# Kernel tuning notes

Measured on AMD Instinct MI355X. Metric: run time of the kernel, lower is better.

Reference implementation:

```python
import jax, jax.numpy as jnp
import numpy as np

TOKENS = 8192
HIDDEN = 6144
NUM_EXPERTS = 768  # n_routed_experts (512) + zero_expert_num (256)
TOP_K = 12
ROUTED_SCALING_FACTOR = 2.5


def setup_inputs() -> dict:
    key = jax.random.key(0)
    k1, k2, k3 = jax.random.split(key, 3)
    hidden_states = jax.random.normal(k1, (TOKENS, HIDDEN), dtype=jnp.float32)
    classifier_weight = jax.random.normal(k2, (NUM_EXPERTS, HIDDEN), dtype=jnp.float32) * (1.0 / np.sqrt(HIDDEN))
    e_score_correction_bias = jax.random.normal(k3, (NUM_EXPERTS,), dtype=jnp.float32) * 0.1
    return {
        "hidden_states": hidden_states,
        "classifier_weight": classifier_weight,
        "e_score_correction_bias": e_score_correction_bias,
    }


def reference(hidden_states, classifier_weight, e_score_correction_bias):
    # [T, H] -> router logits [T, E] in fp32 (source casts to float32)
    x = hidden_states.reshape(-1, HIDDEN).astype(jnp.float32)
    router_logits = jnp.einsum('th,eh->te', x, classifier_weight)

    # npu_moe_gating_top_k(renorm=0, norm_type=0): softmax scores,
    # bias-corrected selection, gather un-biased scores, scale.
    scores = jax.nn.softmax(router_logits, axis=-1)                # [T, E]
    scores_for_choice = scores + e_score_correction_bias[None, :]  # [T, E]
    _, topk_indices = jax.lax.top_k(scores_for_choice, TOP_K)       # [T, K]
    topk_weights = jnp.take_along_axis(scores, topk_indices, axis=-1)
    topk_weights = topk_weights * ROUTED_SCALING_FACTOR

    return topk_indices.astype(jnp.int32), topk_weights
```

## Files before the change

### kernel.cpp

```cpp
#include <hip/hip_runtime.h>

#define TOKENS  8192
#define HIDDEN  6144
#define EXPERTS 768
#define TOPK    12
#define RSF     2.5f
#define ROWH    (HIDDEN * 2)

typedef float    f4 __attribute__((ext_vector_type(4)));
typedef _Float16 h8 __attribute__((ext_vector_type(8)));
typedef _Float16 h2 __attribute__((ext_vector_type(2)));
typedef __fp16   g2 __attribute__((ext_vector_type(2)));

#define BM 128
#define BN 96
#define BK 32
#define NKT (HIDDEN / BK)
#define BUFH 14336
#define LOH  7168
#define LO_SCALE 4096.0f
#define LO_INV   2.44140625e-4f

static __device__ inline h2 pk(float a, float b) {
    g2 r = __builtin_amdgcn_cvt_pkrtz(a, b);
    return __builtin_bit_cast(h2, r);
}

static __device__ inline void cvt8(const f4 a, const f4 b, h8& hi, h8& lo) {
    h2 ha = pk(a.x, a.y), hb = pk(a.z, a.w), hc = pk(b.x, b.y), hd = pk(b.z, b.w);
    h2 la = pk((a.x - (float)ha[0]) * LO_SCALE, (a.y - (float)ha[1]) * LO_SCALE);
    h2 lb = pk((a.z - (float)hb[0]) * LO_SCALE, (a.w - (float)hb[1]) * LO_SCALE);
    h2 lc = pk((b.x - (float)hc[0]) * LO_SCALE, (b.y - (float)hc[1]) * LO_SCALE);
    h2 ld = pk((b.z - (float)hd[0]) * LO_SCALE, (b.w - (float)hd[1]) * LO_SCALE);
    hi[0]=ha[0]; hi[1]=ha[1]; hi[2]=hb[0]; hi[3]=hb[1];
    hi[4]=hc[0]; hi[5]=hc[1]; hi[6]=hd[0]; hi[7]=hd[1];
    lo[0]=la[0]; lo[1]=la[1]; lo[2]=lb[0]; lo[3]=lb[1];
    lo[4]=lc[0]; lo[5]=lc[1]; lo[6]=ld[0]; lo[7]=ld[1];
}

__global__ __launch_bounds__(256)
void split_convert(float* __restrict__ X, float* __restrict__ W) {
    const size_t GX = (size_t)TOKENS * HIDDEN / 8;
    const size_t GW = (size_t)EXPERTS * HIDDEN / 8;
    size_t gid = (size_t)blockIdx.x * 256 + threadIdx.x;
    if (gid >= GX + GW) return;
    float* base; size_t loc;
    if (gid < GX) { base = X; loc = gid; } else { base = W; loc = gid - GX; }
    const f4* p = (const f4*)(base + loc * 8);
    f4 a = p[0], b = p[1];
    h8 hi, lo;
    cvt8(a, b, hi, lo);
    h8* o = (h8*)(base + loc * 8);
    o[0] = hi; o[1] = lo;
}

typedef __attribute__((address_space(1))) const void av1;
typedef __attribute__((address_space(3))) void av3;
static __device__ inline void stage16(const void* g, void* l) {
    __builtin_amdgcn_global_load_lds((av1*)g, (av3*)l, 16, 0, 0);
}

__global__ __launch_bounds__(256, 2)
void router_gemm(const _Float16* __restrict__ Xs, const _Float16* __restrict__ Ws,
                 float* __restrict__ L) {
    __shared__ _Float16 sm[2 * BUFH];

    const int t    = threadIdx.x;
    const int bm   = blockIdx.y * BM;
    const int bn   = blockIdx.x * BN;
    const int lane = t & 63;
    const int w    = t >> 6;
    const int lr   = lane & 15;
    const int lq   = lane >> 4;

    const _Float16* ps[7];
    uint32_t        ldso[7];
#pragma unroll
    for (int q = 0; q < 7; ++q) {
        const int j    = w * 7 + q;
        const int isLo = (j >= 14);
        const int jj   = isLo ? j - 14 : j;
        const int r    = jj * 16 + (lane >> 2);
        const int p    = lane & 3;
        const int g    = p ^ (r & 3);
        const _Float16* row = (r < BM) ? (Xs + (size_t)(bm + r) * ROWH)
                                       : (Ws + (size_t)(bn + r - BM) * ROWH);
        ps[q]   = row + g * 16 + isLo * 8;
        ldso[q] = (uint32_t)(isLo * LOH + jj * 512);
    }

    uint32_t aoff[4], boff[3];
#pragma unroll
    for (int mi = 0; mi < 4; ++mi) {
        const int r = (w & 1) * 64 + mi * 16 + lr;
        aoff[mi] = r * 32 + ((lq ^ (r & 3)) * 8);
    }
#pragma unroll
    for (int ni = 0; ni < 3; ++ni) {
        const int r = 128 + (w >> 1) * 48 + ni * 16 + lr;
        boff[ni] = r * 32 + ((lq ^ (r & 3)) * 8);
    }

    f4 acc_h[4][3], acc_c[4][3];
#pragma unroll
    for (int i = 0; i < 4; ++i)
#pragma unroll
        for (int j = 0; j < 3; ++j) { acc_h[i][j] = f4{0,0,0,0}; acc_c[i][j] = f4{0,0,0,0}; }

#pragma unroll
    for (int q = 0; q < 7; ++q) {
        stage16((const void*)ps[q], (void*)(sm + ldso[q]));
        ps[q] += 64;
    }

    auto do_tile = [&](const uint32_t boR, const uint32_t boW, const bool doStage) {
        if (doStage) {
#pragma unroll
            for (int q = 0; q < 7; ++q) {
                stage16((const void*)ps[q], (void*)(sm + boW + ldso[q]));
                ps[q] += 64;
            }
        }
        h8 ah[4], al[4], bh[3], bl[3];
#pragma unroll
        for (int mi = 0; mi < 4; ++mi) {
            ah[mi] = *(const h8*)(sm + boR + aoff[mi]);
            al[mi] = *(const h8*)(sm + boR + aoff[mi] + LOH);
        }
#pragma unroll
        for (int ni = 0; ni < 3; ++ni) {
            bh[ni] = *(const h8*)(sm + boR + boff[ni]);
            bl[ni] = *(const h8*)(sm + boR + boff[ni] + LOH);
        }
#pragma unroll
        for (int mi = 0; mi < 4; ++mi)
#pragma unroll
            for (int ni = 0; ni < 3; ++ni) {
                acc_h[mi][ni] = __builtin_amdgcn_mfma_f32_16x16x32_f16(ah[mi], bh[ni], acc_h[mi][ni], 0, 0, 0);
                acc_c[mi][ni] = __builtin_amdgcn_mfma_f32_16x16x32_f16(ah[mi], bl[ni], acc_c[mi][ni], 0, 0, 0);
                acc_c[mi][ni] = __builtin_amdgcn_mfma_f32_16x16x32_f16(al[mi], bh[ni], acc_c[mi][ni], 0, 0, 0);
            }
    };

    for (int T2 = 0; T2 < NKT / 2; ++T2) {
        __syncthreads();
        do_tile(0u, (uint32_t)BUFH, true);
        __syncthreads();
        do_tile((uint32_t)BUFH, 0u, T2 != NKT / 2 - 1);
    }

#pragma unroll
    for (int mi = 0; mi < 4; ++mi)
#pragma unroll
        for (int ni = 0; ni < 3; ++ni)
#pragma unroll
            for (int r = 0; r < 4; ++r) {
                const int gm = bm + (w & 1) * 64 + mi * 16 + lq * 4 + r;
                const int gn = bn + (w >> 1) * 48 + ni * 16 + lr;
                L[(size_t)gm * EXPERTS + gn] = acc_h[mi][ni][r] + acc_c[mi][ni][r] * LO_INV;
            }
}

__global__ __launch_bounds__(256)
void router_topk(const float* __restrict__ L, const float* __restrict__ bias,
                 float* __restrict__ outIdx, float* __restrict__ outW) {
    __shared__ float sb[EXPERTS];
    const int t = threadIdx.x;
    for (int i = t; i < EXPERTS; i += 256) sb[i] = bias[i];
    __syncthreads();

    const int lane  = t & 63;
    const int wave  = t >> 6;
    const int token = blockIdx.x * 4 + wave;
    const float* row = L + (size_t)token * EXPERTS;

    float lg[12];
#pragma unroll
    for (int j = 0; j < 12; ++j) lg[j] = row[lane + 64 * j];

    float m = lg[0];
#pragma unroll
    for (int j = 1; j < 12; ++j) m = fmaxf(m, lg[j]);
#pragma unroll
    for (int o = 32; o > 0; o >>= 1) m = fmaxf(m, __shfl_xor(m, o));

    float s = 0.0f;
#pragma unroll
    for (int j = 0; j < 12; ++j) { lg[j] = __expf(lg[j] - m); s += lg[j]; }
#pragma unroll
    for (int o = 32; o > 0; o >>= 1) s += __shfl_xor(s, o);
    const float inv = 1.0f / s;

    float cand[12];
#pragma unroll
    for (int j = 0; j < 12; ++j) {
        lg[j] *= inv;
        cand[j] = lg[j] + sb[lane + 64 * j];
    }

#pragma unroll
    for (int r = 0; r < TOPK; ++r) {
        float bv = -__builtin_inff();
        int   bi = EXPERTS;
#pragma unroll
        for (int j = 0; j < 12; ++j) {
            const int e = lane + 64 * j;
            const bool better = (cand[j] > bv) || (cand[j] == bv && e < bi);
            bv = better ? cand[j] : bv;
            bi = better ? e : bi;
        }
#pragma unroll
        for (int o = 32; o > 0; o >>= 1) {
            const float ov = __shfl_xor(bv, o);
            const int   oi = __shfl_xor(bi, o);
            const bool better = (ov > bv) || (ov == bv && oi < bi);
            bv = better ? ov : bv;
            bi = better ? oi : bi;
        }
        if (lane == 0) {
            outIdx[token * TOPK + r] = (float)bi;
            outW  [token * TOPK + r] = (bv - sb[bi]) * RSF;
        }
        if ((bi & 63) == lane) {
            const int slot = bi >> 6;
#pragma unroll
            for (int j = 0; j < 12; ++j)
                if (j == slot) cand[j] = -__builtin_inff();
        }
    }
}

extern "C" void kernel_launch(void* const* d_in, const int* in_sizes, int n_in,
                              void* d_out, int out_size, void* d_ws, size_t ws_size,
                              hipStream_t stream) {
    float* X = (float*)d_in[0];
    float* W = (float*)d_in[1];
    const float* B = (const float*)d_in[2];

    float* logits = (float*)d_ws;
    float* outIdx = (float*)d_out;
    float* outW   = outIdx + (size_t)TOKENS * TOPK;

    const int ngroups = (TOKENS + EXPERTS) * HIDDEN / 8;
    split_convert<<<ngroups / 256, 256, 0, stream>>>(X, W);

    dim3 grid_gemm(EXPERTS / BN, TOKENS / BM);
    router_gemm<<<grid_gemm, 256, 0, stream>>>((const _Float16*)X, (const _Float16*)W, logits);
    router_topk<<<TOKENS / 4, 256, 0, stream>>>(logits, B, outIdx, outW);
}
```

Before: 544.1 us.

## Load W operand directly to registers, stage only X tile through LDS

The B (weight) fragments are now loaded straight from global memory into registers with double-buffered register prefetch, and only the X tile is staged in LDS. This shrinks the LDS footprint per buffer and the LDS read traffic for B. It also changes the X swizzle to XOR in more row bits to reduce bank conflicts. The trade-off is more VGPR pressure and uncoalesced, per-wave redundant global loads of W, since each wave pair reloads the same rows.

```diff
diff --git a/kernel.cpp b/kernel.cpp
--- a/kernel.cpp
+++ b/kernel.cpp
@@ -16,8 +16,7 @@
 #define BN 96
 #define BK 32
 #define NKT (HIDDEN / BK)
-#define BUFH 14336
-#define LOH  7168
+#define BUFH 8192
 #define LO_SCALE 4096.0f
 #define LO_INV   2.44140625e-4f
 
@@ -73,32 +72,33 @@
     const int lr   = lane & 15;
     const int lq   = lane >> 4;
 
-    const _Float16* ps[7];
-    uint32_t        ldso[7];
-#pragma unroll
-    for (int q = 0; q < 7; ++q) {
-        const int j    = w * 7 + q;
-        const int isLo = (j >= 14);
-        const int jj   = isLo ? j - 14 : j;
+    const _Float16* ps[4];
+    uint32_t        ldso[4];
+#pragma unroll
+    for (int q = 0; q < 4; ++q) {
+        const int i    = w * 4 + q;
+        const int isLo = (i >= 8);
+        const int jj   = i & 7;
         const int r    = jj * 16 + (lane >> 2);
-        const int p    = lane & 3;
-        const int g    = p ^ (r & 3);
-        const _Float16* row = (r < BM) ? (Xs + (size_t)(bm + r) * ROWH)
-                                       : (Ws + (size_t)(bn + r - BM) * ROWH);
-        ps[q]   = row + g * 16 + isLo * 8;
-        ldso[q] = (uint32_t)(isLo * LOH + jj * 512);
-    }
-
-    uint32_t aoff[4], boff[3];
+        const int g    = (lane & 3) ^ (r & 3) ^ ((r >> 2) & 3);
+        ps[q]   = Xs + (size_t)(bm + r) * ROWH + g * 16 + isLo * 8;
+        ldso[q] = (uint32_t)(isLo * 4096 + jj * 512);
+    }
+
+    const _Float16* pb[6];
+#pragma unroll
+    for (int ni = 0; ni < 3; ++ni) {
+        const int row = bn + (w >> 1) * 48 + ni * 16 + lr;
+#pragma unroll
+        for (int e = 0; e < 2; ++e)
+            pb[ni * 2 + e] = Ws + (size_t)row * ROWH + lq * 16 + e * 8;
+    }
+
+    uint32_t aoff[4];
 #pragma unroll
     for (int mi = 0; mi < 4; ++mi) {
         const int r = (w & 1) * 64 + mi * 16 + lr;
-        aoff[mi] = r * 32 + ((lq ^ (r & 3)) * 8);
-    }
-#pragma unroll
-    for (int ni = 0; ni < 3; ++ni) {
-        const int r = 128 + (w >> 1) * 48 + ni * 16 + lr;
-        boff[ni] = r * 32 + ((lq ^ (r & 3)) * 8);
+        aoff[mi] = r * 32 + ((lq ^ (r & 3) ^ ((r >> 2) & 3)) * 8);
     }
 
     f4 acc_h[4][3], acc_c[4][3];
@@ -107,46 +107,54 @@
 #pragma unroll
         for (int j = 0; j < 3; ++j) { acc_h[i][j] = f4{0,0,0,0}; acc_c[i][j] = f4{0,0,0,0}; }
 
-#pragma unroll
-    for (int q = 0; q < 7; ++q) {
+    h8 bcur[6], bnxt[6];
+
+#pragma unroll
+    for (int q = 0; q < 4; ++q) {
         stage16((const void*)ps[q], (void*)(sm + ldso[q]));
         ps[q] += 64;
     }
-
-    auto do_tile = [&](const uint32_t boR, const uint32_t boW, const bool doStage) {
-        if (doStage) {
-#pragma unroll
-            for (int q = 0; q < 7; ++q) {
+#pragma unroll
+    for (int i = 0; i < 6; ++i) {
+        bcur[i] = *(const h8*)pb[i];
+        pb[i] += 64;
+    }
+
+    auto do_tile = [&](const uint32_t boR, const uint32_t boW,
+                       h8* bR, h8* bN, const bool pf) {
+        if (pf) {
+#pragma unroll
+            for (int q = 0; q < 4; ++q) {
                 stage16((const void*)ps[q], (void*)(sm + boW + ldso[q]));
                 ps[q] += 64;
             }
-        }
-        h8 ah[4], al[4], bh[3], bl[3];
+#pragma unroll
+            for (int i = 0; i < 6; ++i) {
+                bN[i] = *(const h8*)pb[i];
+                pb[i] += 64;
+            }
+        }
+        h8 ah[4], al[4];
 #pragma unroll
         for (int mi = 0; mi < 4; ++mi) {
             ah[mi] = *(const h8*)(sm + boR + aoff[mi]);
-            al[mi] = *(const h8*)(sm + boR + aoff[mi] + LOH);
-        }
-#pragma unroll
-        for (int ni = 0; ni < 3; ++ni) {
-            bh[ni] = *(const h8*)(sm + boR + boff[ni]);
-            bl[ni] = *(const h8*)(sm + boR + boff[ni] + LOH);
+            al[mi] = *(const h8*)(sm + boR + aoff[mi] + 4096);
         }
 #pragma unroll
         for (int mi = 0; mi < 4; ++mi)
 #pragma unroll
             for (int ni = 0; ni < 3; ++ni) {
-                acc_h[mi][ni] = __builtin_amdgcn_mfma_f32_16x16x32_f16(ah[mi], bh[ni], acc_h[mi][ni], 0, 0, 0);
-                acc_c[mi][ni] = __builtin_amdgcn_mfma_f32_16x16x32_f16(ah[mi], bl[ni], acc_c[mi][ni], 0, 0, 0);
-                acc_c[mi][ni] = __builtin_amdgcn_mfma_f32_16x16x32_f16(al[mi], bh[ni], acc_c[mi][ni], 0, 0, 0);
+                acc_h[mi][ni] = __builtin_amdgcn_mfma_f32_16x16x32_f16(ah[mi], bR[2*ni],   acc_h[mi][ni], 0, 0, 0);
+                acc_c[mi][ni] = __builtin_amdgcn_mfma_f32_16x16x32_f16(ah[mi], bR[2*ni+1], acc_c[mi][ni], 0, 0, 0);
+                acc_c[mi][ni] = __builtin_amdgcn_mfma_f32_16x16x32_f16(al[mi], bR[2*ni],   acc_c[mi][ni], 0, 0, 0);
             }
     };
 
     for (int T2 = 0; T2 < NKT / 2; ++T2) {
         __syncthreads();
-        do_tile(0u, (uint32_t)BUFH, true);
+        do_tile(0u, (uint32_t)BUFH, bcur, bnxt, true);
         __syncthreads();
-        do_tile((uint32_t)BUFH, 0u, T2 != NKT / 2 - 1);
+        do_tile((uint32_t)BUFH, 0u, bnxt, bcur, T2 != NKT / 2 - 1);
     }
 
 #pragma unroll
```

New measurement: 658.6 us. 21.0% more time.
